# Optimization experiments

Hardware: AMD Instinct MI355X
Metric: run time of the kernel (lower is better)

## Reference

```python
import jax, jax.numpy as jnp
import numpy as np

B, H, W, C = 8, 64, 64, 512
G = 32  # num_groups
EPS = 1e-5


def group_norm(x, scale, bias):
    b, h, w, c = x.shape
    xg = x.reshape(b, h, w, G, c // G)
    mean = jnp.mean(xg, axis=(1, 2, 4), keepdims=True)
    var = jnp.var(xg, axis=(1, 2, 4), keepdims=True)
    xg = (xg - mean) / jnp.sqrt(var + EPS)
    x = xg.reshape(b, h, w, c)
    return x * scale + bias


def conv1x1(x, w, b):
    # NHWC 1x1 conv == channel matmul
    return jnp.einsum('bhwc,cd->bhwd', x, w) + b


def setup_inputs() -> dict:
    key = jax.random.key(0)
    ks = jax.random.split(key, 10)
    init = lambda k, shape: jax.random.normal(k, shape, dtype=jnp.float32) * (1.0 / np.sqrt(C))
    return {
        'x': jax.random.normal(ks[0], (B, H, W, C), dtype=jnp.float32),
        'gn_scale': jnp.ones((C,), dtype=jnp.float32),
        'gn_bias': jnp.zeros((C,), dtype=jnp.float32),
        'wq': init(ks[1], (C, C)), 'bq': jnp.zeros((C,), jnp.float32),
        'wk': init(ks[2], (C, C)), 'bk': jnp.zeros((C,), jnp.float32),
        'wv': init(ks[3], (C, C)), 'bv': jnp.zeros((C,), jnp.float32),
        'wo': init(ks[4], (C, C)), 'bo': jnp.zeros((C,), jnp.float32),
    }


def reference(x, gn_scale, gn_bias, wq, bq, wk, bk, wv, bv, wo, bo):
    h = group_norm(x, gn_scale, gn_bias)
    q = conv1x1(h, wq, bq)
    k = conv1x1(h, wk, bk)
    v = conv1x1(h, wv, bv)
    b, hh, ww, c = h.shape
    n = hh * ww
    q = q.reshape(b, n, c)
    k = k.reshape(b, n, c)
    v = v.reshape(b, n, c)
    scores = jnp.einsum('bqc,bkc->bqk', q, k) * (c ** -0.5)
    attn = jax.nn.softmax(scores, axis=-1)
    out = jnp.einsum('bqk,bkc->bqc', attn, v).reshape(b, hh, ww, c)
    out = conv1x1(out, wo, bo)
    return out + x
```

## Files before the change

### kernel.cpp

```cpp
#include <hip/hip_runtime.h>

typedef __bf16 bfx8 __attribute__((ext_vector_type(8)));
typedef __bf16 bfx4 __attribute__((ext_vector_type(4)));
typedef float  f32x4 __attribute__((ext_vector_type(4)));

#define MFMA16(a,b,c) __builtin_amdgcn_mfma_f32_16x16x32_bf16((a),(b),(c),0,0,0)

static constexpr int BATCH = 8;
static constexpr int NTOK  = 4096;
static constexpr int CH    = 512;
static constexpr float GN_EPS = 1e-5f;
static constexpr float ATT_SCALE = 0.044194173824159216f;

__device__ __forceinline__ void gload16(const void* g, void* l)
{
    __builtin_amdgcn_global_load_lds(
        (const __attribute__((address_space(1))) unsigned int*)g,
        (__attribute__((address_space(3))) unsigned int*)l, 16, 0, 0);
}

__global__ __launch_bounds__(256)
void prep_weights(const float* __restrict__ wq, const float* __restrict__ wk,
                  const float* __restrict__ wv, const float* __restrict__ wo,
                  const float* __restrict__ bq, const float* __restrict__ bk,
                  const float* __restrict__ bv,
                  __bf16* __restrict__ wqkvT, __bf16* __restrict__ woT,
                  float* __restrict__ bqkv)
{
    __shared__ __bf16 t[32][36];
    const int z  = blockIdx.z;
    const float* src = (z == 0) ? wq : (z == 1) ? wk : (z == 2) ? wv : wo;
    const int c0 = blockIdx.x * 32, n0 = blockIdx.y * 32;
    const int tid = threadIdx.x;
    const int r = tid >> 3, c4 = (tid & 7) * 4;

    f32x4 in = *(const f32x4*)&src[(size_t)(c0 + r) * 512 + n0 + c4];
    bfx4 tv;
#pragma unroll
    for (int i = 0; i < 4; ++i) tv[i] = (__bf16)in[i];
    *(bfx4*)&t[r][c4] = tv;
    __syncthreads();
    bfx4 o;
#pragma unroll
    for (int i = 0; i < 4; ++i) o[i] = t[c4 + i][r];
    if (z < 3)
        *(bfx4*)&wqkvT[((size_t)(z * 512 + n0 + r)) * 512 + c0 + c4] = o;
    else
        *(bfx4*)&woT[((size_t)(n0 + r)) * 512 + c0 + c4] = o;

    if (z < 3 && blockIdx.x == 0 && blockIdx.y == 0) {
        const float* bs = (z == 0) ? bq : (z == 1) ? bk : bv;
        bqkv[z * 512 + tid]       = bs[tid];
        bqkv[z * 512 + tid + 256] = bs[tid + 256];
    }
}

__global__ __launch_bounds__(256)
void gn_stats(const float* __restrict__ x, const float* __restrict__ gs,
              const float* __restrict__ gb,
              float* __restrict__ scA, float* __restrict__ biA)
{
    const int g = blockIdx.x, b = blockIdx.y;
    const int tid = threadIdx.x;
    const int half = tid & 1;
    const size_t base = (size_t)b * NTOK * CH + g * 16 + half * 8;

    float sum = 0.f, sumsq = 0.f;
    for (int i = tid; i < 2 * NTOK; i += 256) {
        const int s = i >> 1;
        f32x4 v0 = *(const f32x4*)&x[base + (size_t)s * CH];
        f32x4 v1 = *(const f32x4*)&x[base + (size_t)s * CH + 4];
#pragma unroll
        for (int j = 0; j < 4; ++j) {
            sum += v0[j] + v1[j];
            sumsq += v0[j] * v0[j] + v1[j] * v1[j];
        }
    }
#pragma unroll
    for (int o = 32; o; o >>= 1) { sum += __shfl_down(sum, o); sumsq += __shfl_down(sumsq, o); }
    __shared__ float red[8];
    __shared__ float stats[2];
    const int w = tid >> 6;
    if ((tid & 63) == 0) { red[w] = sum; red[4 + w] = sumsq; }
    __syncthreads();
    if (tid == 0) {
        float s1 = red[0] + red[1] + red[2] + red[3];
        float s2 = red[4] + red[5] + red[6] + red[7];
        float mean = s1 * (1.f / 65536.f);
        float var  = s2 * (1.f / 65536.f) - mean * mean;
        stats[0] = mean; stats[1] = rsqrtf(var + GN_EPS);
    }
    __syncthreads();
    if (tid < 16) {
        const int ch = g * 16 + tid;
        const float sc = gs[ch] * stats[1];
        scA[b * 512 + ch] = sc;
        biA[b * 512 + ch] = gb[ch] - stats[0] * sc;
    }
}

__global__ __launch_bounds__(256)
void gemm_qkv(const float* __restrict__ x, const float* __restrict__ scA,
              const float* __restrict__ biA, const __bf16* __restrict__ Bt,
              const float* __restrict__ bias,
              __bf16* __restrict__ qk, __bf16* __restrict__ vT)
{
    const int bm = blockIdx.x * 128, bn = blockIdx.y * 128;
    const int tid = threadIdx.x;
    const int w = tid >> 6, lane = tid & 63, quad = lane >> 4, l15 = lane & 15;
    const int wm = (w >> 1) * 64, wn = (w & 1) * 64;
    const int brow = bm >> 12;

    __shared__ __attribute__((aligned(16))) __bf16 smem_g[5120 + 2 * 128 * 32];
    __bf16 (*As)[40] = (__bf16(*)[40])smem_g;
    __bf16 (*Bs)[128][32] = (__bf16(*)[128][32])(smem_g + 5120);

    f32x4 acc[4][4];
#pragma unroll
    for (int i = 0; i < 4; ++i)
#pragma unroll
        for (int j = 0; j < 4; ++j) acc[i][j] = (f32x4){0.f, 0.f, 0.f, 0.f};

    const int sr = tid >> 2, scol = (tid & 3) * 8;
    const int brow_l = (lane >> 2);
    const int bcp    = lane & 3;

#pragma unroll
    for (int u = 0; u < 2; ++u) {
        const int row = w * 32 + u * 16 + brow_l;
        gload16(Bt + (size_t)(bn + row) * 512 + ((bcp ^ (row & 3)) * 8),
                &Bs[0][w * 32 + u * 16][0]);
    }
    f32x4 xa0 = *(const f32x4*)&x[(size_t)(bm + sr) * 512 + scol];
    f32x4 xa1 = *(const f32x4*)&x[(size_t)(bm + sr) * 512 + scol + 4];
    f32x4 xb0 = *(const f32x4*)&x[(size_t)(bm + sr + 64) * 512 + scol];
    f32x4 xb1 = *(const f32x4*)&x[(size_t)(bm + sr + 64) * 512 + scol + 4];

    for (int k0 = 0; k0 < 512; k0 += 32) {
        const int cur = (k0 >> 5) & 1;
        __syncthreads();
        {
            const float* scp = scA + brow * 512 + k0 + scol;
            const float* bip = biA + brow * 512 + k0 + scol;
            f32x4 s0v = *(const f32x4*)&scp[0], s1v = *(const f32x4*)&scp[4];
            f32x4 b0v = *(const f32x4*)&bip[0], b1v = *(const f32x4*)&bip[4];
            bfx8 ha, hb;
#pragma unroll
            for (int j = 0; j < 4; ++j) {
                ha[j]     = (__bf16)(xa0[j] * s0v[j] + b0v[j]);
                ha[4 + j] = (__bf16)(xa1[j] * s1v[j] + b1v[j]);
                hb[j]     = (__bf16)(xb0[j] * s0v[j] + b0v[j]);
                hb[4 + j] = (__bf16)(xb1[j] * s1v[j] + b1v[j]);
            }
            *(bfx8*)&As[sr][scol]      = ha;
            *(bfx8*)&As[sr + 64][scol] = hb;
        }
        if (k0 + 32 < 512) {
            const int k1 = k0 + 32;
#pragma unroll
            for (int u = 0; u < 2; ++u) {
                const int row = w * 32 + u * 16 + brow_l;
                gload16(Bt + (size_t)(bn + row) * 512 + k1 + ((bcp ^ (row & 3)) * 8),
                        &Bs[cur ^ 1][w * 32 + u * 16][0]);
            }
            xa0 = *(const f32x4*)&x[(size_t)(bm + sr) * 512 + k1 + scol];
            xa1 = *(const f32x4*)&x[(size_t)(bm + sr) * 512 + k1 + scol + 4];
            xb0 = *(const f32x4*)&x[(size_t)(bm + sr + 64) * 512 + k1 + scol];
            xb1 = *(const f32x4*)&x[(size_t)(bm + sr + 64) * 512 + k1 + scol + 4];
        }
        asm volatile("s_waitcnt lgkmcnt(0)\n\ts_barrier" ::: "memory");

        bfx8 af[4], bfr[4];
#pragma unroll
        for (int mi = 0; mi < 4; ++mi) af[mi] = *(const bfx8*)&As[wm + mi * 16 + l15][quad * 8];
#pragma unroll
        for (int ni = 0; ni < 4; ++ni) {
            const int row = wn + ni * 16 + l15;
            bfr[ni] = *(const bfx8*)&Bs[cur][row][(quad ^ (row & 3)) * 8];
        }
#pragma unroll
        for (int mi = 0; mi < 4; ++mi)
#pragma unroll
            for (int ni = 0; ni < 4; ++ni)
                acc[mi][ni] = MFMA16(af[mi], bfr[ni], acc[mi][ni]);
    }

    if (blockIdx.y < 8) {
        const float scale = (blockIdx.y < 4) ? ATT_SCALE : 1.0f;
#pragma unroll
        for (int ni = 0; ni < 4; ++ni) {
            const int col = bn + wn + ni * 16 + l15;
            const float bv = bias[col];
#pragma unroll
            for (int mi = 0; mi < 4; ++mi)
#pragma unroll
                for (int rr = 0; rr < 4; ++rr) {
                    const int row = bm + wm + mi * 16 + quad * 4 + rr;
                    qk[(size_t)row * 1024 + col] = (__bf16)((acc[mi][ni][rr] + bv) * scale);
                }
        }
    } else {
        const int vch0 = bn - 1024;
        const int tokbase = bm & 4095;
        __bf16* tb = smem_g;
        __syncthreads();
#pragma unroll
        for (int chunk = 0; chunk < 2; ++chunk) {
            if ((w & 1) == chunk) {
#pragma unroll
                for (int ni = 0; ni < 4; ++ni) {
                    const int chc = ni * 16 + l15;
                    const float bv = bias[bn + chunk * 64 + chc];
#pragma unroll
                    for (int mi = 0; mi < 4; ++mi)
#pragma unroll
                        for (int rr = 0; rr < 4; ++rr) {
                            const int tok = wm + mi * 16 + quad * 4 + rr;
                            tb[chc * 136 + tok] = (__bf16)(acc[mi][ni][rr] + bv);
                        }
                }
            }
            __syncthreads();
            {
                const int chn = tid >> 2, t0 = (tid & 3) * 32;
                const size_t gb0 =
                    ((size_t)(brow * 512 + vch0 + chunk * 64 + chn)) * 4096 + tokbase;
#pragma unroll
                for (int u = 0; u < 4; ++u)
                    *(bfx8*)&vT[gb0 + t0 + u * 8] = *(const bfx8*)&tb[chn * 136 + t0 + u * 8];
            }
            __syncthreads();
        }
    }
}

__global__ __launch_bounds__(512, 2)
void attn_fused(const __bf16* __restrict__ qk, const __bf16* __restrict__ vT,
                const __bf16* __restrict__ woT, const float* __restrict__ bo,
                const float* __restrict__ x, float* __restrict__ out)
{
    const int bb = blockIdx.y;
    const int q0 = blockIdx.x * 128;
    const int tid = threadIdx.x;
    const int w = tid >> 6, lane = tid & 63, quad = lane >> 4, l15 = lane & 15;

    __shared__ __attribute__((aligned(16))) unsigned char smem[141312];
    __bf16 (*Ks)[32][512]      = (__bf16(*)[32][512])smem;
    __bf16 (*Vs)[32][4][16][8] = (__bf16(*)[32][4][16][8])(smem + 65536);
    __bf16 (*Ph)[40]           = (__bf16(*)[40])(smem + 131072);
    __bf16 (*Obuf)[520]        = (__bf16(*)[520])smem;

    bfx8 qf[16];
    {
        const __bf16* qptr = qk + ((size_t)(bb * NTOK + q0 + w * 16 + l15)) * 1024;
#pragma unroll
        for (int kk = 0; kk < 16; ++kk)
            qf[kk] = *(const bfx8*)&qptr[kk * 32 + quad * 8];
    }

    f32x4 oacc[32];
#pragma unroll
    for (int i = 0; i < 32; ++i) oacc[i] = (f32x4){0.f, 0.f, 0.f, 0.f};
    float mcur = -1e30f, lcur = 0.f;

#pragma unroll
    for (int u = 0; u < 4; ++u) {
        const int r = w * 4 + u;
        gload16(qk + ((size_t)(bb * NTOK + r)) * 1024 + 512 + ((lane ^ (r & 7)) * 8),
                &Ks[0][r][0]);
    }
#pragma unroll
    for (int u = 0; u < 4; ++u) {
        const int g = w * 4 + u;
        gload16(vT + ((size_t)(bb * 512 + g * 16 + (lane & 15))) * 4096 + (lane >> 4) * 8,
                &Vs[0][g][0][0][0]);
    }

    const int NT = NTOK / 32;
    int buf = 0;
    for (int kt = 0; kt < NT; ++kt) {
        __syncthreads();

        if (kt + 1 < NT) {
            const int kv1 = (kt + 1) * 32;
            const int nb = buf ^ 1;
#pragma unroll
            for (int u = 0; u < 4; ++u) {
                const int r = w * 4 + u;
                gload16(qk + ((size_t)(bb * NTOK + kv1 + r)) * 1024 + 512 + ((lane ^ (r & 7)) * 8),
                        &Ks[nb][r][0]);
            }
#pragma unroll
            for (int u = 0; u < 4; ++u) {
                const int g = w * 4 + u;
                gload16(vT + ((size_t)(bb * 512 + g * 16 + (lane & 15))) * 4096 + kv1 + (lane >> 4) * 8,
                        &Vs[nb][g][0][0][0]);
            }
        }

        f32x4 s0 = (f32x4){0.f, 0.f, 0.f, 0.f}, s1 = (f32x4){0.f, 0.f, 0.f, 0.f};
        __builtin_amdgcn_s_setprio(1);
#pragma unroll
        for (int kk = 0; kk < 16; ++kk) {
            const int pc = (((kk * 4 + quad) ^ (l15 & 7)) * 8);
            bfx8 kb0 = *(const bfx8*)&Ks[buf][l15][pc];
            bfx8 kb1 = *(const bfx8*)&Ks[buf][16 + l15][pc];
            s0 = MFMA16(kb0, qf[kk], s0);
            s1 = MFMA16(kb1, qf[kk], s1);
        }
        __builtin_amdgcn_s_setprio(0);

        float mx = -1e30f;
#pragma unroll
        for (int i = 0; i < 4; ++i) mx = fmaxf(mx, fmaxf(s0[i], s1[i]));
        float ps = 0.f;
        bfx4 pl0, pl1;
#pragma unroll
        for (int i = 0; i < 4; ++i) { float p = __expf(s0[i] - mcur); ps += p; pl0[i] = (__bf16)p; }
#pragma unroll
        for (int i = 0; i < 4; ++i) { float p = __expf(s1[i] - mcur); ps += p; pl1[i] = (__bf16)p; }
        mx = fmaxf(mx, __shfl_xor(mx, 16));
        mx = fmaxf(mx, __shfl_xor(mx, 32));
        if (__builtin_expect(__any(mx > mcur + 8.f), 0)) {
            const float mnew = fmaxf(mcur, mx);
            const float al = __expf(mcur - mnew);
            lcur *= al;
            ps = 0.f;
#pragma unroll
            for (int i = 0; i < 4; ++i) { float p = __expf(s0[i] - mnew); ps += p; pl0[i] = (__bf16)p; }
#pragma unroll
            for (int i = 0; i < 4; ++i) { float p = __expf(s1[i] - mnew); ps += p; pl1[i] = (__bf16)p; }
            mcur = mnew;
#pragma unroll
            for (int ct = 0; ct < 32; ++ct)
#pragma unroll
                for (int r = 0; r < 4; ++r) oacc[ct][r] *= al;
        }

        *(bfx4*)&Ph[w * 16 + l15][quad * 4]      = pl0;
        *(bfx4*)&Ph[w * 16 + l15][16 + quad * 4] = pl1;

        asm volatile("s_waitcnt lgkmcnt(0)" ::: "memory");
        bfx8 pa = *(const bfx8*)&Ph[w * 16 + l15][quad * 8];

        __builtin_amdgcn_s_setprio(1);
#pragma unroll
        for (int ct = 0; ct < 32; ++ct) {
            bfx8 vb = *(const bfx8*)&Vs[buf][ct][quad][l15][0];
            oacc[ct] = MFMA16(vb, pa, oacc[ct]);
        }
        __builtin_amdgcn_s_setprio(0);

        ps += __shfl_xor(ps, 16);
        ps += __shfl_xor(ps, 32);
        lcur += ps;
        buf ^= 1;
    }

#pragma unroll
    for (int h = 0; h < 2; ++h) {
        __syncthreads();
        if ((w >> 2) == h) {
            const float linv = 1.f / lcur;
#pragma unroll
            for (int ct = 0; ct < 32; ++ct) {
                bfx4 ov;
#pragma unroll
                for (int r = 0; r < 4; ++r) ov[r] = (__bf16)(oacc[ct][r] * linv);
                *(bfx4*)&Obuf[(w & 3) * 16 + l15][ct * 16 + quad * 4] = ov;
            }
        }
        __syncthreads();

        const int rs  = (w & 3) * 16;
        const int nt0 = (w >> 2) * 16;
        bfx8 af2[16];
#pragma unroll
        for (int k0 = 0; k0 < 16; ++k0)
            af2[k0] = *(const bfx8*)&Obuf[rs + l15][k0 * 32 + quad * 8];
#pragma unroll 4
        for (int nt = 0; nt < 16; ++nt) {
            f32x4 a2 = (f32x4){0.f, 0.f, 0.f, 0.f};
#pragma unroll
            for (int k0 = 0; k0 < 16; ++k0) {
                bfx8 wb = *(const bfx8*)&woT[(size_t)((nt0 + nt) * 16 + l15) * 512 + k0 * 32 + quad * 8];
                a2 = MFMA16(af2[k0], wb, a2);
            }
            const int col = (nt0 + nt) * 16 + l15;
            const float bv = bo[col];
#pragma unroll
            for (int rr = 0; rr < 4; ++rr) {
                const size_t idx =
                    ((size_t)(bb * NTOK + q0 + h * 64 + rs + quad * 4 + rr)) * 512 + col;
                out[idx] = a2[rr] + bv + x[idx];
            }
        }
    }
}

extern "C" void kernel_launch(void* const* d_in, const int* in_sizes, int n_in,
                              void* d_out, int out_size, void* d_ws, size_t ws_size,
                              hipStream_t stream)
{
    const float* x  = (const float*)d_in[0];
    const float* gs = (const float*)d_in[1];
    const float* gb = (const float*)d_in[2];
    const float* wq = (const float*)d_in[3];
    const float* bq = (const float*)d_in[4];
    const float* wk = (const float*)d_in[5];
    const float* bk = (const float*)d_in[6];
    const float* wv = (const float*)d_in[7];
    const float* bv = (const float*)d_in[8];
    const float* wo = (const float*)d_in[9];
    const float* bo = (const float*)d_in[10];
    float* out = (float*)d_out;

    char* ws = (char*)d_ws;
    __bf16* qk    = (__bf16*)(ws);
    __bf16* vT    = (__bf16*)(ws + 67108864);
    __bf16* wqkvT = (__bf16*)(ws + 100663296);
    __bf16* woT   = (__bf16*)(ws + 102236160);
    float*  bqkv  = (float* )(ws + 102760448);
    float*  scA   = (float* )(ws + 102766592);
    float*  biA   = (float* )(ws + 102782976);

    prep_weights<<<dim3(16, 16, 4), 256, 0, stream>>>(wq, wk, wv, wo, bq, bk, bv,
                                                      wqkvT, woT, bqkv);
    gn_stats<<<dim3(32, BATCH), 256, 0, stream>>>(x, gs, gb, scA, biA);
    gemm_qkv<<<dim3(256, 12), 256, 0, stream>>>(x, scA, biA, wqkvT, bqkv, qk, vT);
    attn_fused<<<dim3(NTOK / 128, BATCH), 512, 0, stream>>>(qk, vT, woT, bo, x, out);
}
```

Measured before the change: 711.6 us.

## Software-pipeline PV MFMA one tile behind QK and pass P via bpermute

Restructures the attention loop so the P·V MFMAs for the previous key tile run right after the current QK^T MFMAs. This interleaves the matrix work with the softmax exp latency. V gets a triple-buffered LDS ring, with a zeroed third slot for the first iteration, and the prefetch wraps around instead of branching. The probabilities are now packed with v_cvt_pk_bf16_f32 and transposed through ds_bpermute rather than an LDS round trip with a waitcnt. The cost is more LDS per block (163840 bytes), which may limit occupancy, plus a redundant wrapped prefetch on the last iteration.

```diff
diff --git a/kernel.cpp b/kernel.cpp
--- a/kernel.cpp
+++ b/kernel.cpp
@@ -17,6 +17,13 @@
     __builtin_amdgcn_global_load_lds(
         (const __attribute__((address_space(1))) unsigned int*)g,
         (__attribute__((address_space(3))) unsigned int*)l, 16, 0, 0);
+}
+
+__device__ __forceinline__ unsigned cvtpk(float lo, float hi)
+{
+    unsigned r;
+    asm("v_cvt_pk_bf16_f32 %0, %1, %2" : "=v"(r) : "v"(lo), "v"(hi));
+    return r;
 }
 
 __global__ __launch_bounds__(256)
@@ -244,11 +251,17 @@
     const int tid = threadIdx.x;
     const int w = tid >> 6, lane = tid & 63, quad = lane >> 4, l15 = lane & 15;
 
-    __shared__ __attribute__((aligned(16))) unsigned char smem[141312];
+    __shared__ __attribute__((aligned(16))) unsigned char smem[163840];
     __bf16 (*Ks)[32][512]      = (__bf16(*)[32][512])smem;
     __bf16 (*Vs)[32][4][16][8] = (__bf16(*)[32][4][16][8])(smem + 65536);
-    __bf16 (*Ph)[40]           = (__bf16(*)[40])(smem + 131072);
     __bf16 (*Obuf)[520]        = (__bf16(*)[520])smem;
+
+    {
+        f32x4 z = (f32x4){0.f, 0.f, 0.f, 0.f};
+        char* vz = (char*)&Vs[2][0][0][0][0] + tid * 64;
+#pragma unroll
+        for (int u = 0; u < 4; ++u) *(f32x4*)(vz + u * 16) = z;
+    }
 
     bfx8 qf[16];
     {
@@ -262,6 +275,7 @@
 #pragma unroll
     for (int i = 0; i < 32; ++i) oacc[i] = (f32x4){0.f, 0.f, 0.f, 0.f};
     float mcur = -1e30f, lcur = 0.f;
+    bfx8 pb = {};
 
 #pragma unroll
     for (int u = 0; u < 4; ++u) {
@@ -272,17 +286,18 @@
 #pragma unroll
     for (int u = 0; u < 4; ++u) {
         const int g = w * 4 + u;
-        gload16(vT + ((size_t)(bb * 512 + g * 16 + (lane & 15))) * 4096 + (lane >> 4) * 8,
+        gload16(vT + ((size_t)(bb * 512 + g * 16 + l15)) * 4096 + quad * 8,
                 &Vs[0][g][0][0][0]);
     }
 
     const int NT = NTOK / 32;
     int buf = 0;
+    int sr = 2, s0m = 0, sw = 1;
     for (int kt = 0; kt < NT; ++kt) {
         __syncthreads();
 
-        if (kt + 1 < NT) {
-            const int kv1 = (kt + 1) * 32;
+        {
+            const int kv1 = ((kt + 1) & (NT - 1)) * 32;
             const int nb = buf ^ 1;
 #pragma unroll
             for (int u = 0; u < 4; ++u) {
@@ -293,8 +308,8 @@
 #pragma unroll
             for (int u = 0; u < 4; ++u) {
                 const int g = w * 4 + u;
-                gload16(vT + ((size_t)(bb * 512 + g * 16 + (lane & 15))) * 4096 + kv1 + (lane >> 4) * 8,
-                        &Vs[nb][g][0][0][0]);
+                gload16(vT + ((size_t)(bb * 512 + g * 16 + l15)) * 4096 + kv1 + quad * 8,
+                        &Vs[sw][g][0][0][0]);
             }
         }
 
@@ -310,15 +325,20 @@
         }
         __builtin_amdgcn_s_setprio(0);
 
+#pragma unroll
+        for (int ct = 0; ct < 32; ++ct) {
+            bfx8 vb = *(const bfx8*)&Vs[sr][ct][quad][l15][0];
+            oacc[ct] = MFMA16(vb, pb, oacc[ct]);
+        }
+
         float mx = -1e30f;
 #pragma unroll
         for (int i = 0; i < 4; ++i) mx = fmaxf(mx, fmaxf(s0[i], s1[i]));
-        float ps = 0.f;
-        bfx4 pl0, pl1;
-#pragma unroll
-        for (int i = 0; i < 4; ++i) { float p = __expf(s0[i] - mcur); ps += p; pl0[i] = (__bf16)p; }
-#pragma unroll
-        for (int i = 0; i < 4; ++i) { float p = __expf(s1[i] - mcur); ps += p; pl1[i] = (__bf16)p; }
+        float pf[8]; float ps = 0.f;
+#pragma unroll
+        for (int i = 0; i < 4; ++i) { pf[i]     = __expf(s0[i] - mcur); ps += pf[i]; }
+#pragma unroll
+        for (int i = 0; i < 4; ++i) { pf[4 + i] = __expf(s1[i] - mcur); ps += pf[4 + i]; }
         mx = fmaxf(mx, __shfl_xor(mx, 16));
         mx = fmaxf(mx, __shfl_xor(mx, 32));
         if (__builtin_expect(__any(mx > mcur + 8.f), 0)) {
@@ -327,9 +347,9 @@
             lcur *= al;
             ps = 0.f;
 #pragma unroll
-            for (int i = 0; i < 4; ++i) { float p = __expf(s0[i] - mnew); ps += p; pl0[i] = (__bf16)p; }
-#pragma unroll
-            for (int i = 0; i < 4; ++i) { float p = __expf(s1[i] - mnew); ps += p; pl1[i] = (__bf16)p; }
+            for (int i = 0; i < 4; ++i) { pf[i]     = __expf(s0[i] - mnew); ps += pf[i]; }
+#pragma unroll
+            for (int i = 0; i < 4; ++i) { pf[4 + i] = __expf(s1[i] - mnew); ps += pf[4 + i]; }
             mcur = mnew;
 #pragma unroll
             for (int ct = 0; ct < 32; ++ct)
@@ -337,24 +357,42 @@
                 for (int r = 0; r < 4; ++r) oacc[ct][r] *= al;
         }
 
-        *(bfx4*)&Ph[w * 16 + l15][quad * 4]      = pl0;
-        *(bfx4*)&Ph[w * 16 + l15][16 + quad * 4] = pl1;
-
-        asm volatile("s_waitcnt lgkmcnt(0)" ::: "memory");
-        bfx8 pa = *(const bfx8*)&Ph[w * 16 + l15][quad * 8];
-
-        __builtin_amdgcn_s_setprio(1);
-#pragma unroll
-        for (int ct = 0; ct < 32; ++ct) {
-            bfx8 vb = *(const bfx8*)&Vs[buf][ct][quad][l15][0];
-            oacc[ct] = MFMA16(vb, pa, oacc[ct]);
-        }
-        __builtin_amdgcn_s_setprio(0);
+        {
+            unsigned pk0a = cvtpk(pf[0], pf[1]);
+            unsigned pk0b = cvtpk(pf[2], pf[3]);
+            unsigned pk1a = cvtpk(pf[4], pf[5]);
+            unsigned pk1b = cvtpk(pf[6], pf[7]);
+            const int bpA = ((((lane & 16) << 1) | l15)) << 2;
+            const int bpB = bpA + 64;
+            int t0a = __builtin_amdgcn_ds_bpermute(bpA, (int)pk0a);
+            int t1a = __builtin_amdgcn_ds_bpermute(bpA, (int)pk1a);
+            int t0b = __builtin_amdgcn_ds_bpermute(bpA, (int)pk0b);
+            int t1b = __builtin_amdgcn_ds_bpermute(bpA, (int)pk1b);
+            int u0a = __builtin_amdgcn_ds_bpermute(bpB, (int)pk0a);
+            int u1a = __builtin_amdgcn_ds_bpermute(bpB, (int)pk1a);
+            int u0b = __builtin_amdgcn_ds_bpermute(bpB, (int)pk0b);
+            int u1b = __builtin_amdgcn_ds_bpermute(bpB, (int)pk1b);
+            const bool lo = lane < 32;
+            union { int i[4]; bfx8 v; } pbu;
+            pbu.i[0] = lo ? t0a : t1a;
+            pbu.i[1] = lo ? t0b : t1b;
+            pbu.i[2] = lo ? u0a : u1a;
+            pbu.i[3] = lo ? u0b : u1b;
+            pb = pbu.v;
+        }
 
         ps += __shfl_xor(ps, 16);
         ps += __shfl_xor(ps, 32);
         lcur += ps;
+
         buf ^= 1;
+        const int t = sr; sr = s0m; s0m = sw; sw = t;
+    }
+
+#pragma unroll
+    for (int ct = 0; ct < 32; ++ct) {
+        bfx8 vb = *(const bfx8*)&Vs[sr][ct][quad][l15][0];
+        oacc[ct] = MFMA16(vb, pb, oacc[ct]);
     }
 
 #pragma unroll
```

Result: slower. 1.776 ms (+149.6%).
